# Kernel optimization log

Measured on AMD Instinct MI355X. Metric: run time of the kernel, lower is better.

## Reference

```python
import jax, jax.numpy as jnp
import numpy as np

I, H, O, T = 64, 512, 1, 65536


def setup_inputs() -> dict:
    key = jax.random.key(0)
    ks = jax.random.split(key, 12)
    s = 1.0 / np.sqrt(H)
    u = lambda k, shape: jax.random.uniform(k, shape, jnp.float32, -s, s)
    return {
        "input_seq": jax.random.normal(ks[0], (T, I), jnp.float32),
        "W_ih1": u(ks[1], (4 * H, I)), "W_hh1": u(ks[2], (4 * H, H)),
        "b_ih1": u(ks[3], (4 * H,)), "b_hh1": u(ks[4], (4 * H,)),
        "W_ih2": u(ks[5], (4 * H, H)), "W_hh2": u(ks[6], (4 * H, H)),
        "b_ih2": u(ks[7], (4 * H,)), "b_hh2": u(ks[8], (4 * H,)),
        "W_out": u(ks[9], (O, H)), "b_out": u(ks[10], (O,)),
    }


def _lstm_cell(x, h, c, W_ih, W_hh, b_ih, b_hh):
    # torch.nn.LSTMCell gate order: input, forget, cell(g), output
    gates = x @ W_ih.T + b_ih + h @ W_hh.T + b_hh  # [4H]
    i, f, g, o = jnp.split(gates, 4)
    c_new = jax.nn.sigmoid(f) * c + jax.nn.sigmoid(i) * jnp.tanh(g)
    h_new = jax.nn.sigmoid(o) * jnp.tanh(c_new)
    return h_new, c_new


def reference(input_seq, W_ih1, W_hh1, b_ih1, b_hh1,
              W_ih2, W_hh2, b_ih2, b_hh2, W_out, b_out):
    h = input_seq.dtype
    zeros = jnp.zeros((H,), h)

    def step(carry, x_t):
        h1, c1, h2, c2 = carry
        h1, c1 = _lstm_cell(x_t, h1, c1, W_ih1, W_hh1, b_ih1, b_hh1)
        h2, c2 = _lstm_cell(h1, h2, c2, W_ih2, W_hh2, b_ih2, b_hh2)
        return (h1, c1, h2, c2), None

    (h1, c1, h2, c2), _ = jax.lax.scan(step, (zeros, zeros, zeros, zeros), input_seq)
    # final output = linear(last h2), as in the original forward
    return h2 @ W_out.T + b_out
```

## Files before the change

kernel.cpp:

```cpp
#include <hip/hip_runtime.h>

#define IDIM  64
#define HDIM  512
#define T_LEN 65536
#define NWG   128
#define NTHR  512

__device__ unsigned long long g_h1[2][HDIM];
__device__ unsigned long long g_h2[2][HDIM];

__device__ __forceinline__ unsigned long long pack(float v, int k) {
  return ((unsigned long long)(unsigned)k << 32) | (unsigned long long)__float_as_uint(v);
}

__global__ void lstm_init() {
  int t = threadIdx.x;
  for (int e = t; e < HDIM; e += blockDim.x) {
    g_h1[0][e] = 0xFFFFFFFF00000000ull;
    g_h1[1][e] = 0xFFFFFFFF00000000ull;
    g_h2[0][e] = 0xFFFFFFFF00000000ull;
    g_h2[1][e] = 0x0000000000000000ull;
  }
}

__global__ __launch_bounds__(NTHR)
__attribute__((amdgpu_waves_per_eu(2, 2)))
void lstm_main(
    const float* __restrict__ x_seq,
    const float* __restrict__ W_ih1, const float* __restrict__ W_hh1,
    const float* __restrict__ b_ih1, const float* __restrict__ b_hh1,
    const float* __restrict__ W_ih2, const float* __restrict__ W_hh2,
    const float* __restrict__ b_ih2, const float* __restrict__ b_hh2,
    const float* __restrict__ W_out, const float* __restrict__ b_out,
    float* __restrict__ out)
{
  const int wg   = blockIdx.x;
  const int tid  = threadIdx.x;
  const int wave = tid >> 6;
  const int role = wave >> 2;
  const int lane = tid & 63;
  const int g    = lane >> 4;
  const int s    = lane & 15;
  const int j    = wg * 4 + (wave & 3);
  const int r    = g * HDIM + j;

  float w[64];
  if (role == 0) {
#pragma unroll
    for (int m = 0; m < 36; ++m) {
      int e = s * 36 + m;
      w[m] = (e < HDIM) ? W_hh1[(size_t)r * HDIM + e]
                        : W_ih1[(size_t)r * IDIM + (e - HDIM)];
    }
#pragma unroll
    for (int m = 0; m < 36; ++m) asm volatile("" : "+v"(w[m]));
  } else {
#pragma unroll
    for (int c = 0; c < 16; ++c) {
#pragma unroll
      for (int i = 0; i < 4; ++i) {
        int er = s * 64 + ((c + s) & 15) * 4 + i;
        w[c * 4 + i] = (er < HDIM) ? W_ih2[(size_t)r * HDIM + er]
                                   : W_hh2[(size_t)r * HDIM + (er - HDIM)];
      }
    }
#pragma unroll
    for (int m = 0; m < 64; ++m) asm volatile("" : "+v"(w[m]));
  }
  const float bsel = (role == 0) ? (b_ih1[r] + b_hh1[r]) : (b_ih2[r] + b_hh2[r]);

  float cst = 0.f;
  int bud = 1 << 24;

  __shared__ __align__(16) float vec[2][HDIM + IDIM + HDIM];

  for (int k = 0; k <= T_LEN; ++k) {
    const unsigned expect = (unsigned)(k - 1);
    const int p1  = (k + 1) & 1;
    const int p2  = k & 1;
    const int buf = k & 1;

    float xv = 0.f;
    if (tid < IDIM && k < T_LEN) xv = x_seq[(size_t)k * IDIM + tid];

    unsigned long long a = 0, b = 0;
    bool ok1 = false, ok2 = false;
    do {
      if (!ok1) {
        a = __hip_atomic_load(&g_h1[p1][tid], __ATOMIC_RELAXED, __HIP_MEMORY_SCOPE_AGENT);
        ok1 = ((unsigned)(a >> 32) == expect);
      }
      if (!ok2) {
        b = __hip_atomic_load(&g_h2[p2][tid], __ATOMIC_RELAXED, __HIP_MEMORY_SCOPE_AGENT);
        ok2 = ((unsigned)(b >> 32) == expect);
      }
    } while ((!ok1 || !ok2) && --bud > 0);

    vec[buf][tid] = __uint_as_float((unsigned)a);
    vec[buf][HDIM + IDIM + tid] = __uint_as_float((unsigned)b);
    if (tid < IDIM) vec[buf][HDIM + tid] = xv;
    __syncthreads();

    const bool active = (role == 0) ? (k < T_LEN) : (k > 0);
    if (active) {
      float acc = 0.f;
      if (role == 0) {
#pragma unroll
        for (int mc = 0; mc < 9; ++mc) {
          const float4 hv = *reinterpret_cast<const float4*>(&vec[buf][s * 36 + mc * 4]);
          acc = fmaf(w[mc * 4 + 0], hv.x, acc);
          acc = fmaf(w[mc * 4 + 1], hv.y, acc);
          acc = fmaf(w[mc * 4 + 2], hv.z, acc);
          acc = fmaf(w[mc * 4 + 3], hv.w, acc);
        }
      } else {
        const int vb = (s < 8) ? 0 : IDIM;
#pragma unroll
        for (int c = 0; c < 16; ++c) {
          const int off = s * 64 + ((c + s) & 15) * 4 + vb;
          const float4 hv = *reinterpret_cast<const float4*>(&vec[buf][off]);
          acc = fmaf(w[c * 4 + 0], hv.x, acc);
          acc = fmaf(w[c * 4 + 1], hv.y, acc);
          acc = fmaf(w[c * 4 + 2], hv.z, acc);
          acc = fmaf(w[c * 4 + 3], hv.w, acc);
        }
      }
      acc += __shfl_xor(acc, 8, 16);
      acc += __shfl_xor(acc, 4, 16);
      acc += __shfl_xor(acc, 2, 16);
      acc += __shfl_xor(acc, 1, 16);

      const float xs  = acc + bsel;
      const float xin = (g == 2) ? 2.f * xs : xs;
      const float sgm = 1.f / (1.f + expf(-xin));
      const float act = (g == 2) ? 2.f * sgm - 1.f : sgm;
      const float ai = __shfl(act, 0, 64);
      const float af = __shfl(act, 16, 64);
      const float ag = __shfl(act, 32, 64);
      const float ao = __shfl(act, 48, 64);
      cst = af * cst + ai * ag;
      const float tc = 2.f / (1.f + expf(-2.f * cst)) - 1.f;
      const float hv = ao * tc;
      if (lane == 0) {
        if (role == 0)
          __hip_atomic_store(&g_h1[k & 1][j], pack(hv, k),
                             __ATOMIC_RELAXED, __HIP_MEMORY_SCOPE_AGENT);
        else
          __hip_atomic_store(&g_h2[(k + 1) & 1][j], pack(hv, k),
                             __ATOMIC_RELAXED, __HIP_MEMORY_SCOPE_AGENT);
      }
    }
  }

  if (wg == 0 && wave == 0) {
    float acc = 0.f;
    int bud2 = 1 << 24;
#pragma unroll
    for (int e = 0; e < HDIM / 64; ++e) {
      const int idx = lane + e * 64;
      unsigned long long u;
      do {
        u = __hip_atomic_load(&g_h2[1][idx], __ATOMIC_RELAXED, __HIP_MEMORY_SCOPE_AGENT);
      } while ((unsigned)(u >> 32) != (unsigned)T_LEN && --bud2 > 0);
      acc = fmaf(W_out[idx], __uint_as_float((unsigned)u), acc);
    }
    acc += __shfl_xor(acc, 32, 64);
    acc += __shfl_xor(acc, 16, 64);
    acc += __shfl_xor(acc, 8, 64);
    acc += __shfl_xor(acc, 4, 64);
    acc += __shfl_xor(acc, 2, 64);
    acc += __shfl_xor(acc, 1, 64);
    if (lane == 0) out[0] = acc + b_out[0];
  }
}

extern "C" void kernel_launch(void* const* d_in, const int* in_sizes, int n_in,
                              void* d_out, int out_size, void* d_ws, size_t ws_size,
                              hipStream_t stream) {
  const float* x_seq = (const float*)d_in[0];
  const float* W_ih1 = (const float*)d_in[1];
  const float* W_hh1 = (const float*)d_in[2];
  const float* b_ih1 = (const float*)d_in[3];
  const float* b_hh1 = (const float*)d_in[4];
  const float* W_ih2 = (const float*)d_in[5];
  const float* W_hh2 = (const float*)d_in[6];
  const float* b_ih2 = (const float*)d_in[7];
  const float* b_hh2 = (const float*)d_in[8];
  const float* W_out = (const float*)d_in[9];
  const float* b_out = (const float*)d_in[10];
  float* out = (float*)d_out;

  hipLaunchKernelGGL(lstm_init, dim3(1), dim3(256), 0, stream);
  hipLaunchKernelGGL(lstm_main, dim3(NWG), dim3(NTHR), 0, stream,
                     x_seq, W_ih1, W_hh1, b_ih1, b_hh1,
                     W_ih2, W_hh2, b_ih2, b_hh2, W_out, b_out, out);
}
```

Before: 129.3 ms.

## Dedicate a poller wave per workgroup and merge h1/h2 flag buffers

Adds a ninth wave per workgroup that alone spins on the global h1/h2 flags, loads x, and fills the shared vector, while the eight compute waves only wait on __syncthreads. The two global state arrays are merged into one double-buffered array indexed by the step parity, so one poll covers both layers. The intent is to take polling latency and global-load traffic off the compute waves and to cut contention on the flag lines. It raises occupancy to three waves per EU and puts every step's critical path through a single wave doing 16 loads per lane.

```diff
diff --git a/kernel.cpp b/kernel.cpp
--- a/kernel.cpp
+++ b/kernel.cpp
@@ -4,10 +4,9 @@
 #define HDIM  512
 #define T_LEN 65536
 #define NWG   128
-#define NTHR  512
-
-__device__ unsigned long long g_h1[2][HDIM];
-__device__ unsigned long long g_h2[2][HDIM];
+#define NTHR  576
+
+__device__ unsigned long long g_hh[2][2 * HDIM];
 
 __device__ __forceinline__ unsigned long long pack(float v, int k) {
   return ((unsigned long long)(unsigned)k << 32) | (unsigned long long)__float_as_uint(v);
@@ -16,15 +15,15 @@
 __global__ void lstm_init() {
   int t = threadIdx.x;
   for (int e = t; e < HDIM; e += blockDim.x) {
-    g_h1[0][e] = 0xFFFFFFFF00000000ull;
-    g_h1[1][e] = 0xFFFFFFFF00000000ull;
-    g_h2[0][e] = 0xFFFFFFFF00000000ull;
-    g_h2[1][e] = 0x0000000000000000ull;
+    g_hh[1][e]        = 0xFFFFFFFF00000000ull;
+    g_hh[0][e]        = 0xFFFFFFFE00000000ull;
+    g_hh[1][HDIM + e] = 0xFFFFFFFF00000000ull;
+    g_hh[0][HDIM + e] = 0x0000000000000000ull;
   }
 }
 
 __global__ __launch_bounds__(NTHR)
-__attribute__((amdgpu_waves_per_eu(2, 2)))
+__attribute__((amdgpu_waves_per_eu(3, 3)))
 void lstm_main(
     const float* __restrict__ x_seq,
     const float* __restrict__ W_ih1, const float* __restrict__ W_hh1,
@@ -37,11 +36,71 @@
   const int wg   = blockIdx.x;
   const int tid  = threadIdx.x;
   const int wave = tid >> 6;
-  const int role = wave >> 2;
   const int lane = tid & 63;
+
+  __shared__ __align__(16) float vec[2][HDIM + IDIM + HDIM];
+
+  if (wave == 0) {
+    int bud = 1 << 24;
+    for (int k = 0; k <= T_LEN; ++k) {
+      const unsigned expect = (unsigned)(k - 1);
+      const int pb  = (k + 1) & 1;
+      const int buf = k & 1;
+      float xv = 0.f;
+      if (k < T_LEN) xv = x_seq[(size_t)k * IDIM + lane];
+
+      unsigned long long v[16];
+      bool allok;
+      do {
+#pragma unroll
+        for (int i = 0; i < 16; ++i)
+          v[i] = __hip_atomic_load(&g_hh[pb][lane + 64 * i],
+                                   __ATOMIC_RELAXED, __HIP_MEMORY_SCOPE_AGENT);
+        bool ok = true;
+#pragma unroll
+        for (int i = 0; i < 16; ++i) ok &= ((unsigned)(v[i] >> 32) == expect);
+        allok = __all(ok);
+      } while (!allok && --bud > 0);
+
+#pragma unroll
+      for (int i = 0; i < 16; ++i) {
+        const int slot = lane + 64 * i;
+        const int dst  = (slot < HDIM) ? slot : slot + IDIM;
+        vec[buf][dst] = __uint_as_float((unsigned)v[i]);
+      }
+      vec[buf][HDIM + lane] = xv;
+      __syncthreads();
+    }
+
+    if (wg == 0) {
+      float acc = 0.f;
+      int bud2 = 1 << 24;
+#pragma unroll
+      for (int e = 0; e < HDIM / 64; ++e) {
+        const int idx = lane + e * 64;
+        unsigned long long u;
+        do {
+          u = __hip_atomic_load(&g_hh[0][HDIM + idx],
+                                __ATOMIC_RELAXED, __HIP_MEMORY_SCOPE_AGENT);
+        } while ((unsigned)(u >> 32) != (unsigned)T_LEN && --bud2 > 0);
+        acc = fmaf(W_out[idx], __uint_as_float((unsigned)u), acc);
+      }
+      acc += __shfl_xor(acc, 32, 64);
+      acc += __shfl_xor(acc, 16, 64);
+      acc += __shfl_xor(acc, 8, 64);
+      acc += __shfl_xor(acc, 4, 64);
+      acc += __shfl_xor(acc, 2, 64);
+      acc += __shfl_xor(acc, 1, 64);
+      if (lane == 0) out[0] = acc + b_out[0];
+    }
+    return;
+  }
+
+  const int cw   = wave - 1;
+  const int role = cw >> 2;
   const int g    = lane >> 4;
   const int s    = lane & 15;
-  const int j    = wg * 4 + (wave & 3);
+  const int j    = wg * 4 + (cw & 3);
   const int r    = g * HDIM + j;
 
   float w[64];
@@ -70,35 +129,9 @@
   const float bsel = (role == 0) ? (b_ih1[r] + b_hh1[r]) : (b_ih2[r] + b_hh2[r]);
 
   float cst = 0.f;
-  int bud = 1 << 24;
-
-  __shared__ __align__(16) float vec[2][HDIM + IDIM + HDIM];
 
   for (int k = 0; k <= T_LEN; ++k) {
-    const unsigned expect = (unsigned)(k - 1);
-    const int p1  = (k + 1) & 1;
-    const int p2  = k & 1;
     const int buf = k & 1;
-
-    float xv = 0.f;
-    if (tid < IDIM && k < T_LEN) xv = x_seq[(size_t)k * IDIM + tid];
-
-    unsigned long long a = 0, b = 0;
-    bool ok1 = false, ok2 = false;
-    do {
-      if (!ok1) {
-        a = __hip_atomic_load(&g_h1[p1][tid], __ATOMIC_RELAXED, __HIP_MEMORY_SCOPE_AGENT);
-        ok1 = ((unsigned)(a >> 32) == expect);
-      }
-      if (!ok2) {
-        b = __hip_atomic_load(&g_h2[p2][tid], __ATOMIC_RELAXED, __HIP_MEMORY_SCOPE_AGENT);
-        ok2 = ((unsigned)(b >> 32) == expect);
-      }
-    } while ((!ok1 || !ok2) && --bud > 0);
-
-    vec[buf][tid] = __uint_as_float((unsigned)a);
-    vec[buf][HDIM + IDIM + tid] = __uint_as_float((unsigned)b);
-    if (tid < IDIM) vec[buf][HDIM + tid] = xv;
     __syncthreads();
 
     const bool active = (role == 0) ? (k < T_LEN) : (k > 0);
@@ -142,35 +175,11 @@
       const float tc = 2.f / (1.f + expf(-2.f * cst)) - 1.f;
       const float hv = ao * tc;
       if (lane == 0) {
-        if (role == 0)
-          __hip_atomic_store(&g_h1[k & 1][j], pack(hv, k),
-                             __ATOMIC_RELAXED, __HIP_MEMORY_SCOPE_AGENT);
-        else
-          __hip_atomic_store(&g_h2[(k + 1) & 1][j], pack(hv, k),
-                             __ATOMIC_RELAXED, __HIP_MEMORY_SCOPE_AGENT);
-      }
-    }
-  }
-
-  if (wg == 0 && wave == 0) {
-    float acc = 0.f;
-    int bud2 = 1 << 24;
-#pragma unroll
-    for (int e = 0; e < HDIM / 64; ++e) {
-      const int idx = lane + e * 64;
-      unsigned long long u;
-      do {
-        u = __hip_atomic_load(&g_h2[1][idx], __ATOMIC_RELAXED, __HIP_MEMORY_SCOPE_AGENT);
-      } while ((unsigned)(u >> 32) != (unsigned)T_LEN && --bud2 > 0);
-      acc = fmaf(W_out[idx], __uint_as_float((unsigned)u), acc);
-    }
-    acc += __shfl_xor(acc, 32, 64);
-    acc += __shfl_xor(acc, 16, 64);
-    acc += __shfl_xor(acc, 8, 64);
-    acc += __shfl_xor(acc, 4, 64);
-    acc += __shfl_xor(acc, 2, 64);
-    acc += __shfl_xor(acc, 1, 64);
-    if (lane == 0) out[0] = acc + b_out[0];
+        const int vidx = (role == 0) ? j : (HDIM + j);
+        __hip_atomic_store(&g_hh[k & 1][vidx], pack(hv, k),
+                           __ATOMIC_RELAXED, __HIP_MEMORY_SCOPE_AGENT);
+      }
+    }
   }
 }
 
```

Measured after the change: 254.1 ms. 1.96x slower.

## Split LSTM layers onto separate workgroups with ring-buffered decoupled pipeline

Applied to the files above, without the earlier changes.

Workgroups now specialise by layer: the first 64 run only layer 1 and the other 64 only layer 2, each with 8 waves per unit. Layer 1 writes into a 4-deep ring buffer and runs ahead of layer 2, held back by a per-workgroup progress counter, so the two recurrences no longer wait on one shared per-step barrier. This takes layer 2's latency off layer 1's critical path and vice versa. In exchange there is extra progress polling, and each workgroup now carries eight hidden units instead of four.

```diff
diff --git a/kernel.cpp b/kernel.cpp
--- a/kernel.cpp
+++ b/kernel.cpp
@@ -5,9 +5,11 @@
 #define T_LEN 65536
 #define NWG   128
 #define NTHR  512
-
-__device__ unsigned long long g_h1[2][HDIM];
-__device__ unsigned long long g_h2[2][HDIM];
+#define RD    4
+
+__device__ unsigned long long g_r1[RD][HDIM];
+__device__ unsigned long long g_r2[2][HDIM];
+__device__ long long g_prog[64];
 
 __device__ __forceinline__ unsigned long long pack(float v, int k) {
   return ((unsigned long long)(unsigned)k << 32) | (unsigned long long)__float_as_uint(v);
@@ -16,11 +18,12 @@
 __global__ void lstm_init() {
   int t = threadIdx.x;
   for (int e = t; e < HDIM; e += blockDim.x) {
-    g_h1[0][e] = 0xFFFFFFFF00000000ull;
-    g_h1[1][e] = 0xFFFFFFFF00000000ull;
-    g_h2[0][e] = 0xFFFFFFFF00000000ull;
-    g_h2[1][e] = 0x0000000000000000ull;
+    g_r1[RD - 1][e] = 0xFFFFFFFF00000000ull;
+    for (int d = 0; d < RD - 1; ++d) g_r1[d][e] = 0xFFFFFFFE00000000ull;
+    g_r2[1][e] = 0xFFFFFFFF00000000ull;
+    g_r2[0][e] = 0xFFFFFFFE00000000ull;
   }
+  if (t < 64) g_prog[t] = -1;
 }
 
 __global__ __launch_bounds__(NTHR)
@@ -37,99 +40,68 @@
   const int wg   = blockIdx.x;
   const int tid  = threadIdx.x;
   const int wave = tid >> 6;
-  const int role = wave >> 2;
   const int lane = tid & 63;
   const int g    = lane >> 4;
   const int s    = lane & 15;
-  const int j    = wg * 4 + (wave & 3);
-  const int r    = g * HDIM + j;
-
-  float w[64];
-  if (role == 0) {
+
+  __shared__ __align__(16) float vec[2][2 * HDIM];
+  int bud = 1 << 24;
+
+  if (wg < 64) {
+    const int j = wg * 8 + wave;
+    const int r = g * HDIM + j;
+    float wa[36];
 #pragma unroll
     for (int m = 0; m < 36; ++m) {
       int e = s * 36 + m;
-      w[m] = (e < HDIM) ? W_hh1[(size_t)r * HDIM + e]
-                        : W_ih1[(size_t)r * IDIM + (e - HDIM)];
-    }
-#pragma unroll
-    for (int m = 0; m < 36; ++m) asm volatile("" : "+v"(w[m]));
-  } else {
-#pragma unroll
-    for (int c = 0; c < 16; ++c) {
-#pragma unroll
-      for (int i = 0; i < 4; ++i) {
-        int er = s * 64 + ((c + s) & 15) * 4 + i;
-        w[c * 4 + i] = (er < HDIM) ? W_ih2[(size_t)r * HDIM + er]
-                                   : W_hh2[(size_t)r * HDIM + (er - HDIM)];
-      }
-    }
-#pragma unroll
-    for (int m = 0; m < 64; ++m) asm volatile("" : "+v"(w[m]));
-  }
-  const float bsel = (role == 0) ? (b_ih1[r] + b_hh1[r]) : (b_ih2[r] + b_hh2[r]);
-
-  float cst = 0.f;
-  int bud = 1 << 24;
-
-  __shared__ __align__(16) float vec[2][HDIM + IDIM + HDIM];
-
-  for (int k = 0; k <= T_LEN; ++k) {
-    const unsigned expect = (unsigned)(k - 1);
-    const int p1  = (k + 1) & 1;
-    const int p2  = k & 1;
-    const int buf = k & 1;
-
-    float xv = 0.f;
-    if (tid < IDIM && k < T_LEN) xv = x_seq[(size_t)k * IDIM + tid];
-
-    unsigned long long a = 0, b = 0;
-    bool ok1 = false, ok2 = false;
-    do {
-      if (!ok1) {
-        a = __hip_atomic_load(&g_h1[p1][tid], __ATOMIC_RELAXED, __HIP_MEMORY_SCOPE_AGENT);
-        ok1 = ((unsigned)(a >> 32) == expect);
-      }
-      if (!ok2) {
-        b = __hip_atomic_load(&g_h2[p2][tid], __ATOMIC_RELAXED, __HIP_MEMORY_SCOPE_AGENT);
-        ok2 = ((unsigned)(b >> 32) == expect);
-      }
-    } while ((!ok1 || !ok2) && --bud > 0);
-
-    vec[buf][tid] = __uint_as_float((unsigned)a);
-    vec[buf][HDIM + IDIM + tid] = __uint_as_float((unsigned)b);
-    if (tid < IDIM) vec[buf][HDIM + tid] = xv;
-    __syncthreads();
-
-    const bool active = (role == 0) ? (k < T_LEN) : (k > 0);
-    if (active) {
+      wa[m] = (e < HDIM) ? W_hh1[(size_t)r * HDIM + e]
+                         : W_ih1[(size_t)r * IDIM + (e - HDIM)];
+    }
+#pragma unroll
+    for (int m = 0; m < 36; ++m) asm volatile("" : "+v"(wa[m]));
+    const float bsel = b_ih1[r] + b_hh1[r];
+    float cst = 0.f;
+
+    for (int k = 0; k < T_LEN; ++k) {
+      const int buf = k & 1;
+      const unsigned expect = (unsigned)(k - 1);
+      const long long kd = (long long)k - RD;
+
+      float xv = 0.f;
+      if (tid < IDIM) xv = x_seq[(size_t)k * IDIM + tid];
+
+      unsigned long long a = 0;
+      bool ok1 = false, okp = (tid >= 64);
+      do {
+        if (!ok1) {
+          a = __hip_atomic_load(&g_r1[(k + RD - 1) % RD][tid],
+                                __ATOMIC_RELAXED, __HIP_MEMORY_SCOPE_AGENT);
+          ok1 = ((unsigned)(a >> 32) == expect);
+        }
+        if (!okp) {
+          long long p = __hip_atomic_load(&g_prog[tid],
+                                          __ATOMIC_RELAXED, __HIP_MEMORY_SCOPE_AGENT);
+          okp = (p >= kd);
+        }
+      } while ((!ok1 || !okp) && --bud > 0);
+
+      vec[buf][tid] = __uint_as_float((unsigned)a);
+      if (tid < IDIM) vec[buf][HDIM + tid] = xv;
+      __syncthreads();
+
       float acc = 0.f;
-      if (role == 0) {
-#pragma unroll
-        for (int mc = 0; mc < 9; ++mc) {
-          const float4 hv = *reinterpret_cast<const float4*>(&vec[buf][s * 36 + mc * 4]);
-          acc = fmaf(w[mc * 4 + 0], hv.x, acc);
-          acc = fmaf(w[mc * 4 + 1], hv.y, acc);
-          acc = fmaf(w[mc * 4 + 2], hv.z, acc);
-          acc = fmaf(w[mc * 4 + 3], hv.w, acc);
-        }
-      } else {
-        const int vb = (s < 8) ? 0 : IDIM;
-#pragma unroll
-        for (int c = 0; c < 16; ++c) {
-          const int off = s * 64 + ((c + s) & 15) * 4 + vb;
-          const float4 hv = *reinterpret_cast<const float4*>(&vec[buf][off]);
-          acc = fmaf(w[c * 4 + 0], hv.x, acc);
-          acc = fmaf(w[c * 4 + 1], hv.y, acc);
-          acc = fmaf(w[c * 4 + 2], hv.z, acc);
-          acc = fmaf(w[c * 4 + 3], hv.w, acc);
-        }
+#pragma unroll
+      for (int mc = 0; mc < 9; ++mc) {
+        const float4 hv = *reinterpret_cast<const float4*>(&vec[buf][s * 36 + mc * 4]);
+        acc = fmaf(wa[mc * 4 + 0], hv.x, acc);
+        acc = fmaf(wa[mc * 4 + 1], hv.y, acc);
+        acc = fmaf(wa[mc * 4 + 2], hv.z, acc);
+        acc = fmaf(wa[mc * 4 + 3], hv.w, acc);
       }
       acc += __shfl_xor(acc, 8, 16);
       acc += __shfl_xor(acc, 4, 16);
       acc += __shfl_xor(acc, 2, 16);
       acc += __shfl_xor(acc, 1, 16);
-
       const float xs  = acc + bsel;
       const float xin = (g == 2) ? 2.f * xs : xs;
       const float sgm = 1.f / (1.f + expf(-xin));
@@ -140,37 +112,108 @@
       const float ao = __shfl(act, 48, 64);
       cst = af * cst + ai * ag;
       const float tc = 2.f / (1.f + expf(-2.f * cst)) - 1.f;
-      const float hv = ao * tc;
-      if (lane == 0) {
-        if (role == 0)
-          __hip_atomic_store(&g_h1[k & 1][j], pack(hv, k),
-                             __ATOMIC_RELAXED, __HIP_MEMORY_SCOPE_AGENT);
-        else
-          __hip_atomic_store(&g_h2[(k + 1) & 1][j], pack(hv, k),
-                             __ATOMIC_RELAXED, __HIP_MEMORY_SCOPE_AGENT);
-      }
-    }
-  }
-
-  if (wg == 0 && wave == 0) {
-    float acc = 0.f;
-    int bud2 = 1 << 24;
-#pragma unroll
-    for (int e = 0; e < HDIM / 64; ++e) {
-      const int idx = lane + e * 64;
-      unsigned long long u;
+      const float hv1 = ao * tc;
+      if (lane == 0)
+        __hip_atomic_store(&g_r1[k % RD][j], pack(hv1, k),
+                           __ATOMIC_RELAXED, __HIP_MEMORY_SCOPE_AGENT);
+    }
+  } else {
+    const int w2 = wg - 64;
+    const int j  = w2 * 8 + wave;
+    const int r  = g * HDIM + j;
+    float wb[64];
+#pragma unroll
+    for (int c = 0; c < 16; ++c) {
+#pragma unroll
+      for (int i = 0; i < 4; ++i) {
+        int er = s * 64 + ((c + s) & 15) * 4 + i;
+        wb[c * 4 + i] = (er < HDIM) ? W_ih2[(size_t)r * HDIM + er]
+                                    : W_hh2[(size_t)r * HDIM + (er - HDIM)];
+      }
+    }
+#pragma unroll
+    for (int m = 0; m < 64; ++m) asm volatile("" : "+v"(wb[m]));
+    const float bsel = b_ih2[r] + b_hh2[r];
+    float cst = 0.f;
+
+    for (int m = 0; m < T_LEN; ++m) {
+      const int buf = m & 1;
+      const unsigned ex1 = (unsigned)m;
+      const unsigned ex2 = (unsigned)(m - 1);
+
+      unsigned long long a = 0, b = 0;
+      bool ok1 = false, ok2 = false;
       do {
-        u = __hip_atomic_load(&g_h2[1][idx], __ATOMIC_RELAXED, __HIP_MEMORY_SCOPE_AGENT);
-      } while ((unsigned)(u >> 32) != (unsigned)T_LEN && --bud2 > 0);
-      acc = fmaf(W_out[idx], __uint_as_float((unsigned)u), acc);
-    }
-    acc += __shfl_xor(acc, 32, 64);
-    acc += __shfl_xor(acc, 16, 64);
-    acc += __shfl_xor(acc, 8, 64);
-    acc += __shfl_xor(acc, 4, 64);
-    acc += __shfl_xor(acc, 2, 64);
-    acc += __shfl_xor(acc, 1, 64);
-    if (lane == 0) out[0] = acc + b_out[0];
+        if (!ok1) {
+          a = __hip_atomic_load(&g_r1[m % RD][tid],
+                                __ATOMIC_RELAXED, __HIP_MEMORY_SCOPE_AGENT);
+          ok1 = ((unsigned)(a >> 32) == ex1);
+        }
+        if (!ok2) {
+          b = __hip_atomic_load(&g_r2[(m + 1) & 1][tid],
+                                __ATOMIC_RELAXED, __HIP_MEMORY_SCOPE_AGENT);
+          ok2 = ((unsigned)(b >> 32) == ex2);
+        }
+      } while ((!ok1 || !ok2) && --bud > 0);
+
+      vec[buf][tid]        = __uint_as_float((unsigned)a);
+      vec[buf][HDIM + tid] = __uint_as_float((unsigned)b);
+      __syncthreads();
+      if (tid == 0)
+        __hip_atomic_store(&g_prog[w2], (long long)m,
+                           __ATOMIC_RELAXED, __HIP_MEMORY_SCOPE_AGENT);
+
+      float acc = 0.f;
+#pragma unroll
+      for (int c = 0; c < 16; ++c) {
+        const int off = s * 64 + ((c + s) & 15) * 4;
+        const float4 hv = *reinterpret_cast<const float4*>(&vec[buf][off]);
+        acc = fmaf(wb[c * 4 + 0], hv.x, acc);
+        acc = fmaf(wb[c * 4 + 1], hv.y, acc);
+        acc = fmaf(wb[c * 4 + 2], hv.z, acc);
+        acc = fmaf(wb[c * 4 + 3], hv.w, acc);
+      }
+      acc += __shfl_xor(acc, 8, 16);
+      acc += __shfl_xor(acc, 4, 16);
+      acc += __shfl_xor(acc, 2, 16);
+      acc += __shfl_xor(acc, 1, 16);
+      const float xs  = acc + bsel;
+      const float xin = (g == 2) ? 2.f * xs : xs;
+      const float sgm = 1.f / (1.f + expf(-xin));
+      const float act = (g == 2) ? 2.f * sgm - 1.f : sgm;
+      const float ai = __shfl(act, 0, 64);
+      const float af = __shfl(act, 16, 64);
+      const float ag = __shfl(act, 32, 64);
+      const float ao = __shfl(act, 48, 64);
+      cst = af * cst + ai * ag;
+      const float tc = 2.f / (1.f + expf(-2.f * cst)) - 1.f;
+      const float hv2 = ao * tc;
+      if (lane == 0)
+        __hip_atomic_store(&g_r2[m & 1][j], pack(hv2, m),
+                           __ATOMIC_RELAXED, __HIP_MEMORY_SCOPE_AGENT);
+    }
+
+    if (w2 == 0 && wave == 0) {
+      float acc = 0.f;
+      int bud2 = 1 << 24;
+#pragma unroll
+      for (int e = 0; e < HDIM / 64; ++e) {
+        const int idx = lane + e * 64;
+        unsigned long long u;
+        do {
+          u = __hip_atomic_load(&g_r2[1][idx],
+                                __ATOMIC_RELAXED, __HIP_MEMORY_SCOPE_AGENT);
+        } while ((unsigned)(u >> 32) != (unsigned)(T_LEN - 1) && --bud2 > 0);
+        acc = fmaf(W_out[idx], __uint_as_float((unsigned)u), acc);
+      }
+      acc += __shfl_xor(acc, 32, 64);
+      acc += __shfl_xor(acc, 16, 64);
+      acc += __shfl_xor(acc, 8, 64);
+      acc += __shfl_xor(acc, 4, 64);
+      acc += __shfl_xor(acc, 2, 64);
+      acc += __shfl_xor(acc, 1, 64);
+      if (lane == 0) out[0] = acc + b_out[0];
+    }
   }
 }
 
```

Result: slower. 183.0 ms (+41.5%).
